# Optimization experiments

Hardware: AMD Instinct MI355X
Metric: run time of the kernel (lower is better)

Reference implementation:

```python
import math
import jax, jax.numpy as jnp
import numpy as np

B, S, DM, H, KH = 2, 2048, 1024, 16, 4
HD = DM // H          # 64
N_REP = H // KH       # 4
ROPE_THETA = 10000.0


def setup_inputs() -> dict:
    key = jax.random.key(0)
    ks = jax.random.split(key, 5)
    x = jax.random.normal(ks[0], (B, S, DM), dtype=jnp.float32)
    wq = jax.random.normal(ks[1], (H * HD, DM), dtype=jnp.float32) * 0.02
    wk = jax.random.normal(ks[2], (KH * HD, DM), dtype=jnp.float32) * 0.02
    wv = jax.random.normal(ks[3], (KH * HD, DM), dtype=jnp.float32) * 0.02
    wo = jax.random.normal(ks[4], (DM, H * HD), dtype=jnp.float32) * 0.02
    # freqs_cis = exp(i * t * theta^(-2j/d)) represented as cos/sin, shape [S, HD//2]
    inv_freq = 1.0 / (ROPE_THETA ** (jnp.arange(0, HD, 2, dtype=jnp.float32) / HD))
    angles = jnp.arange(S, dtype=jnp.float32)[:, None] * inv_freq[None, :]
    return {
        'x': x, 'wq': wq, 'wk': wk, 'wv': wv, 'wo': wo,
        'freqs_cos': jnp.cos(angles), 'freqs_sin': jnp.sin(angles),
    }


def _rope(t, cos, sin):
    # t: [B, S, h, HD]; pairs (even, odd) rotated as complex mul
    tr = t.reshape(*t.shape[:-1], HD // 2, 2)
    xr, xi = tr[..., 0], tr[..., 1]
    c = cos[None, :, None, :]  # [1, S, 1, HD//2]
    s = sin[None, :, None, :]
    out = jnp.stack([xr * c - xi * s, xr * s + xi * c], axis=-1)
    return out.reshape(t.shape)


def reference(x, wq, wk, wv, wo, freqs_cos, freqs_sin):
    b, s, _ = x.shape
    xq = (x @ wq.T).reshape(b, s, H, HD)
    xk = (x @ wk.T).reshape(b, s, KH, HD)
    xv = (x @ wv.T).reshape(b, s, KH, HD)
    xq = _rope(xq, freqs_cos, freqs_sin)
    xk = _rope(xk, freqs_cos, freqs_sin)
    # [B, h, S, HD]
    xq = xq.transpose(0, 2, 1, 3)
    xk = xk.transpose(0, 2, 1, 3)
    xv = xv.transpose(0, 2, 1, 3)
    # GQA: repeat_interleave kv heads to match query heads
    xk = jnp.repeat(xk, N_REP, axis=1)
    xv = jnp.repeat(xv, N_REP, axis=1)
    scale = 1.0 / math.sqrt(HD)
    scores = jnp.einsum('bhqd,bhkd->bhqk', xq, xk) * scale
    causal = jnp.tril(jnp.ones((s, s), dtype=bool))
    scores = jnp.where(causal[None, None], scores, jnp.finfo(scores.dtype).min)
    attn = jax.nn.softmax(scores, axis=-1)
    out = jnp.einsum('bhqk,bhkd->bhqd', attn, xv)
    out = out.transpose(0, 2, 1, 3).reshape(b, s, H * HD)
    return out @ wo.T
```

## Files before the change

### kernel.cpp

```cpp
#include <hip/hip_runtime.h>
#include <hip/hip_bf16.h>
#include <type_traits>

#define B_ 2
#define S_ 2048
#define DM_ 1024
#define H_ 16
#define KH_ 4
#define HD_ 64
#define NREP_ 4
#define QKV_LD 1536
#define CLOG 0.1803368801111244f
#define FIXM 8.0f

typedef float f32x4 __attribute__((ext_vector_type(4)));
typedef float f32x16 __attribute__((ext_vector_type(16)));
typedef short s16x8 __attribute__((ext_vector_type(8)));
typedef unsigned int u32x2 __attribute__((ext_vector_type(2)));

static __device__ __forceinline__ float bf2f(unsigned short u) {
  union { unsigned int u; float f; } x; x.u = ((unsigned int)u) << 16; return x.f;
}
static __device__ __forceinline__ unsigned short f2bf(float f) {
  union { float f; unsigned int u; } x; x.f = f;
  unsigned int r = (x.u + 0x7fffu + ((x.u >> 16) & 1u)) >> 16;
  return (unsigned short)r;
}
static __device__ __forceinline__ unsigned int cvtpk_bf16(float lo, float hi) {
  unsigned int r;
  asm("v_cvt_pk_bf16_f32 %0, %1, %2" : "=v"(r) : "v"(lo), "v"(hi));
  return r;
}
static __device__ __forceinline__ float fexp2(float x) {
  float r;
  asm("v_exp_f32 %0, %1" : "=v"(r) : "v"(x));
  return r;
}

__device__ __forceinline__ void gload_lds16(const unsigned short* g, unsigned short* l) {
  __builtin_amdgcn_global_load_lds(
      (const __attribute__((address_space(1))) unsigned int*)g,
      (__attribute__((address_space(3))) unsigned int*)l, 16, 0, 0);
}

__global__ void cvt_all_k(const float* __restrict__ x,
                          const float* __restrict__ wq, const float* __restrict__ wk,
                          const float* __restrict__ wv, const float* __restrict__ wo,
                          unsigned short* __restrict__ xb,
                          unsigned short* __restrict__ wqkv, unsigned short* __restrict__ wob) {
  int i = (blockIdx.x * 256 + threadIdx.x) * 4;
  const float* src; unsigned short* dst; int off;
  if (i < 4194304)      { src = x;  dst = xb;              off = i; }
  else if (i < 5242880) { src = wq; dst = wqkv;            off = i - 4194304; }
  else if (i < 5505024) { src = wk; dst = wqkv + 1048576;  off = i - 5242880; }
  else if (i < 5767168) { src = wv; dst = wqkv + 1310720;  off = i - 5505024; }
  else                  { src = wo; dst = wob;             off = i - 5767168; }
  float4 v = *(const float4*)(src + off);
  ushort4 o;
  o.x = f2bf(v.x); o.y = f2bf(v.y); o.z = f2bf(v.z); o.w = f2bf(v.w);
  *(ushort4*)(dst + off) = o;
}

#define BM 128
#define BN 128
#define BK 32

template <typename OT>
__global__ __launch_bounds__(512) void gemm_bt(const unsigned short* __restrict__ A,
                                               const unsigned short* __restrict__ Bw,
                                               OT* __restrict__ C,
                                               int M, int N, int K) {
  __shared__ unsigned short lds_a[BM * BK];
  __shared__ unsigned short lds_b[BN * BK];
  const int tid = threadIdx.x;
  const int wave = tid >> 6, lane = tid & 63;
  const int lr = lane & 15, lg = lane >> 4;
  const int m0 = blockIdx.y * BM, n0 = blockIdx.x * BN;
  const int wr = wave >> 2, wc = wave & 3;

  f32x4 acc[4][2] = {};

  const int srow = tid >> 2, scol = (tid & 3) << 3;

  for (int k0 = 0; k0 < K; k0 += BK) {
    gload_lds16(A + (size_t)(m0 + srow) * K + k0 + scol, &lds_a[tid * 8]);
    gload_lds16(Bw + (size_t)(n0 + srow) * K + k0 + scol, &lds_b[tid * 8]);
    __syncthreads();
    s16x8 af[4], bfr[2];
    #pragma unroll
    for (int mi = 0; mi < 4; ++mi)
      af[mi] = *(const s16x8*)&lds_a[(wr * 64 + mi * 16 + lr) * BK + lg * 8];
    #pragma unroll
    for (int ni = 0; ni < 2; ++ni)
      bfr[ni] = *(const s16x8*)&lds_b[(wc * 32 + ni * 16 + lr) * BK + lg * 8];
    #pragma unroll
    for (int mi = 0; mi < 4; ++mi) {
      #pragma unroll
      for (int ni = 0; ni < 2; ++ni)
        acc[mi][ni] = __builtin_amdgcn_mfma_f32_16x16x32_bf16(af[mi], bfr[ni], acc[mi][ni], 0, 0, 0);
    }
    __syncthreads();
  }
  #pragma unroll
  for (int mi = 0; mi < 4; ++mi) {
    #pragma unroll
    for (int ni = 0; ni < 2; ++ni) {
      #pragma unroll
      for (int r = 0; r < 4; ++r) {
        int row = m0 + wr * 64 + mi * 16 + lg * 4 + r;
        int col = n0 + wc * 32 + ni * 16 + lr;
        if constexpr (std::is_same<OT, unsigned short>::value)
          C[(size_t)row * N + col] = f2bf(acc[mi][ni][r]);
        else
          C[(size_t)row * N + col] = acc[mi][ni][r];
      }
    }
  }
}

__global__ void kvpack_k(const unsigned short* __restrict__ qkv,
                         const float* __restrict__ fc, const float* __restrict__ fs,
                         unsigned short* __restrict__ kp, unsigned short* __restrict__ vp) {
  int idx = blockIdx.x * 256 + threadIdx.x;
  int lane = idx & 63;
  int f  = (idx >> 6) & 3;
  int t  = (idx >> 8) & 63;
  int p  = idx >> 14;
  int b = p >> 2, kh = p & 3;
  int ql = lane & 31, hi = lane >> 5;
  {
    int s = t * 32 + ql;
    int d0 = f * 16 + hi * 8;
    const unsigned short* src = qkv + (size_t)(b * S_ + s) * QKV_LD + 1024 + kh * HD_ + d0;
    s16x8 v = *(const s16x8*)src;
    int i0 = d0 >> 1;
    float4 c4 = *(const float4*)(fc + s * 32 + i0);
    float4 s4 = *(const float4*)(fs + s * 32 + i0);
    float cc[4] = {c4.x, c4.y, c4.z, c4.w};
    float ss[4] = {s4.x, s4.y, s4.z, s4.w};
    union { s16x8 v; unsigned int w[4]; } o;
    #pragma unroll
    for (int e = 0; e < 4; ++e) {
      float xr = bf2f((unsigned short)v[2 * e]);
      float xi = bf2f((unsigned short)v[2 * e + 1]);
      o.w[e] = cvtpk_bf16(xr * cc[e] - xi * ss[e], xr * ss[e] + xi * cc[e]);
    }
    *(s16x8*)(kp + (size_t)idx * 8) = o.v;
  }
  {
    int d = (f >> 1) * 32 + ql;
    int kv0 = t * 32 + (f & 1) * 16 + hi * 8;
    const unsigned short* src = qkv + (size_t)(b * S_ + kv0) * QKV_LD + 1280 + kh * HD_ + d;
    s16x8 o;
    #pragma unroll
    for (int e = 0; e < 8; ++e) o[e] = (short)src[(size_t)e * QKV_LD];
    *(s16x8*)(vp + (size_t)idx * 8) = o;
  }
}

__global__ __launch_bounds__(256, 4) void attn_fwd13(const unsigned short* __restrict__ qkv,
                                                     const unsigned short* __restrict__ kp,
                                                     const unsigned short* __restrict__ vp,
                                                     const float* __restrict__ fc,
                                                     const float* __restrict__ fs,
                                                     unsigned short* __restrict__ ob) {
  __shared__ float mbuf[64][34];
  const int tid = threadIdx.x;
  const int wave = tid >> 6, lane = tid & 63;
  const int ql = lane & 31;
  const int hi = lane >> 5;
  const int bi = blockIdx.x;
  const int xcd = bi & 7;
  const int b = xcd >> 2, kh = xcd & 3;
  const int j = bi >> 3;
  const int h = kh * NREP_ + (j & 3);
  const int bt = j >> 2;

  int c, t0, t1;
  bool typeA = false, paired = false, doOut;
  if (bt < 32) {
    typeA = true; paired = true;
    c = 63 - bt;
    int T = c + 1;
    t0 = (wave * T) >> 2; t1 = ((wave + 1) * T) >> 2;
    doOut = (wave == 0);
  } else if (bt < 40) {
    paired = true;
    int bb2 = bt - 32;
    c = (wave < 2) ? (16 + bb2) : (31 - bb2);
    int T = c + 1, Th = T >> 1;
    if ((wave & 1) == 0) { t0 = 0;  t1 = Th; } else { t0 = Th; t1 = T; }
    doOut = (wave == 0) || (wave == 2);
  } else {
    c = (bt - 40) * 4 + wave;
    t0 = 0; t1 = c + 1;
    doOut = true;
  }
  const int q = c * 32 + ql;

  const unsigned short* qrow = qkv + (size_t)(b * S_ + q) * QKV_LD + h * HD_;
  s16x8 qf[4];
  #pragma unroll
  for (int ks = 0; ks < 4; ++ks) {
    s16x8 v = *(const s16x8*)(qrow + ks * 16 + hi * 8);
    int i0 = ks * 8 + hi * 4;
    float4 c4 = *(const float4*)(fc + q * 32 + i0);
    float4 s4 = *(const float4*)(fs + q * 32 + i0);
    float cc[4] = {c4.x, c4.y, c4.z, c4.w};
    float ss[4] = {s4.x, s4.y, s4.z, s4.w};
    union { s16x8 v; unsigned int w[4]; } o;
    #pragma unroll
    for (int e = 0; e < 4; ++e) {
      float xr = bf2f((unsigned short)v[2 * e]);
      float xi = bf2f((unsigned short)v[2 * e + 1]);
      o.w[e] = cvtpk_bf16(xr * cc[e] - xi * ss[e], xr * ss[e] + xi * cc[e]);
    }
    qf[ks] = o.v;
  }

  const unsigned short* kpt = kp + ((size_t)(b * KH_ + kh) << 17) + lane * 8;
  const unsigned short* vpt = vp + ((size_t)(b * KH_ + kh) << 17) + lane * 8;

  f32x16 oT0 = {};
  f32x16 oT1 = {};
  float l = 0.f;

  s16x8 ka[4], va[4];

#define LOADK(T) do { \
    const unsigned short* kp_ = kpt + ((size_t)(T) << 11); \
    ka[0] = *(const s16x8*)(kp_);        ka[1] = *(const s16x8*)(kp_ + 512); \
    ka[2] = *(const s16x8*)(kp_ + 1024); ka[3] = *(const s16x8*)(kp_ + 1536); \
  } while (0)
#define LOADV(T) do { \
    const unsigned short* vp_ = vpt + ((size_t)(T) << 11); \
    va[0] = *(const s16x8*)(vp_);        va[1] = *(const s16x8*)(vp_ + 512); \
    va[2] = *(const s16x8*)(vp_ + 1024); va[3] = *(const s16x8*)(vp_ + 1536); \
  } while (0)

  LOADK(t0);
  LOADV(t0);
  for (int t = t0; t < t1; ++t) {
    const bool diag = (t == c);
    const bool more = (t + 1 < t1);
    f32x16 st = {};
    __builtin_amdgcn_s_setprio(1);
    st = __builtin_amdgcn_mfma_f32_32x32x16_bf16(ka[0], qf[0], st, 0, 0, 0);
    st = __builtin_amdgcn_mfma_f32_32x32x16_bf16(ka[1], qf[1], st, 0, 0, 0);
    st = __builtin_amdgcn_mfma_f32_32x32x16_bf16(ka[2], qf[2], st, 0, 0, 0);
    st = __builtin_amdgcn_mfma_f32_32x32x16_bf16(ka[3], qf[3], st, 0, 0, 0);
    __builtin_amdgcn_s_setprio(0);
    if (more) LOADK(t + 1);
    if (diag) {
      #pragma unroll
      for (int r = 0; r < 16; ++r)
        if (((r & 3) + 8 * (r >> 2) + 4 * hi) > ql) st[r] = -1e30f;
    }
    #pragma unroll
    for (int ksv = 0; ksv < 2; ++ksv) {
      float pr[8];
      #pragma unroll
      for (int e = 0; e < 8; ++e)
        pr[e] = fexp2(fmaf(st[ksv * 8 + e], CLOG, -FIXM));
      l += ((pr[0] + pr[1]) + (pr[2] + pr[3])) + ((pr[4] + pr[5]) + (pr[6] + pr[7]));
      unsigned int a01 = cvtpk_bf16(pr[0], pr[1]);
      unsigned int a23 = cvtpk_bf16(pr[2], pr[3]);
      unsigned int b45 = cvtpk_bf16(pr[4], pr[5]);
      unsigned int b67 = cvtpk_bf16(pr[6], pr[7]);
      asm volatile("v_permlane32_swap_b32 %0, %1" : "+v"(a01), "+v"(b45));
      asm volatile("v_permlane32_swap_b32 %0, %1" : "+v"(a23), "+v"(b67));
      union { s16x8 v; unsigned int w[4]; } pb;
      pb.w[0] = a01; pb.w[1] = a23; pb.w[2] = b45; pb.w[3] = b67;
      __builtin_amdgcn_s_setprio(1);
      oT0 = __builtin_amdgcn_mfma_f32_32x32x16_bf16(va[ksv], pb.v, oT0, 0, 0, 0);
      oT1 = __builtin_amdgcn_mfma_f32_32x32x16_bf16(va[2 + ksv], pb.v, oT1, 0, 0, 0);
      __builtin_amdgcn_s_setprio(0);
    }
    if (more) LOADV(t + 1);
  }
#undef LOADK
#undef LOADV

#define WRITEP do { float* mp_ = &mbuf[lane][0]; \
    _Pragma("unroll") for (int r = 0; r < 16; ++r) { mp_[r] = oT0[r]; mp_[16 + r] = oT1[r]; } \
    mp_[32] = l; } while (0)
#define MERGEP do { float* mp_ = &mbuf[lane][0]; \
    l += mp_[32]; \
    _Pragma("unroll") for (int r = 0; r < 16; ++r) { \
      oT0[r] += mp_[r]; \
      oT1[r] += mp_[16 + r]; } } while (0)

  __syncthreads();
  if (paired && wave == 1) WRITEP;
  __syncthreads();
  if (paired && wave == 0) MERGEP;
  __syncthreads();
  if (paired && wave == 3) WRITEP;
  __syncthreads();
  if (paired && wave == 2) MERGEP;
  __syncthreads();
  if (typeA && wave == 2) WRITEP;
  __syncthreads();
  if (typeA && wave == 0) MERGEP;
#undef WRITEP
#undef MERGEP

  if (doOut) {
    float l_tot = l + __shfl_xor(l, 32);
    float invl = 1.0f / l_tot;
    unsigned short* orow = ob + (size_t)(b * S_ + q) * DM_ + h * HD_;
    #pragma unroll
    for (int dblk = 0; dblk < 2; ++dblk) {
      #pragma unroll
      for (int g = 0; g < 4; ++g) {
        float e0 = (dblk ? oT1[4 * g + 0] : oT0[4 * g + 0]) * invl;
        float e1 = (dblk ? oT1[4 * g + 1] : oT0[4 * g + 1]) * invl;
        float e2 = (dblk ? oT1[4 * g + 2] : oT0[4 * g + 2]) * invl;
        float e3 = (dblk ? oT1[4 * g + 3] : oT0[4 * g + 3]) * invl;
        u32x2 w;
        w.x = cvtpk_bf16(e0, e1);
        w.y = cvtpk_bf16(e2, e3);
        *(u32x2*)(orow + dblk * 32 + g * 8 + 4 * hi) = w;
      }
    }
  }
}

extern "C" void kernel_launch(void* const* d_in, const int* in_sizes, int n_in,
                              void* d_out, int out_size, void* d_ws, size_t ws_size,
                              hipStream_t stream) {
  const float* x  = (const float*)d_in[0];
  const float* wq = (const float*)d_in[1];
  const float* wk = (const float*)d_in[2];
  const float* wv = (const float*)d_in[3];
  const float* wo = (const float*)d_in[4];
  const float* fc = (const float*)d_in[5];
  const float* fs = (const float*)d_in[6];
  float* out = (float*)d_out;

  const size_t nX    = (size_t)B_ * S_ * DM_;
  const size_t nWQKV = (size_t)QKV_LD * DM_;
  const size_t nWO   = (size_t)DM_ * DM_;
  const size_t nQKV  = (size_t)B_ * S_ * QKV_LD;
  const size_t nKV   = (size_t)B_ * S_ * KH_ * HD_;

  unsigned short* xb    = (unsigned short*)d_ws;
  unsigned short* wqkv  = xb + nX;
  unsigned short* wob   = wqkv + nWQKV;
  unsigned short* qkv   = wob + nWO;
  unsigned short* kpk   = qkv + nQKV;
  unsigned short* vpk   = kpk + nKV;
  unsigned short* a_buf = vpk + nKV;

  const int M = B_ * S_;

  cvt_all_k<<<6656, 256, 0, stream>>>(x, wq, wk, wv, wo, xb, wqkv, wob);

  gemm_bt<unsigned short><<<dim3(QKV_LD / BN, M / BM), 512, 0, stream>>>(
      xb, wqkv, qkv, M, QKV_LD, DM_);

  kvpack_k<<<512, 256, 0, stream>>>(qkv, fc, fs, kpk, vpk);

  attn_fwd13<<<1408, 256, 0, stream>>>(qkv, kpk, vpk, fc, fs, a_buf);

  gemm_bt<float><<<dim3(DM_ / BN, M / BM), 512, 0, stream>>>(
      a_buf, wob, out, M, DM_, DM_);
}
```

Before: 99.52 us.

## Double-buffer GEMM tiles and process two query heads per attention block

```diff
diff --git a/kernel.cpp b/kernel.cpp
--- a/kernel.cpp
+++ b/kernel.cpp
@@ -61,54 +61,64 @@
   *(ushort4*)(dst + off) = o;
 }
 
-#define BM 128
+#define BM 64
 #define BN 128
 #define BK 32
 
 template <typename OT>
-__global__ __launch_bounds__(512) void gemm_bt(const unsigned short* __restrict__ A,
+__global__ __launch_bounds__(256) void gemm_bt(const unsigned short* __restrict__ A,
                                                const unsigned short* __restrict__ Bw,
                                                OT* __restrict__ C,
                                                int M, int N, int K) {
-  __shared__ unsigned short lds_a[BM * BK];
-  __shared__ unsigned short lds_b[BN * BK];
+  __shared__ unsigned short lds_a[2][BM * BK];
+  __shared__ unsigned short lds_b[2][BN * BK];
   const int tid = threadIdx.x;
   const int wave = tid >> 6, lane = tid & 63;
   const int lr = lane & 15, lg = lane >> 4;
   const int m0 = blockIdx.y * BM, n0 = blockIdx.x * BN;
-  const int wr = wave >> 2, wc = wave & 3;
-
-  f32x4 acc[4][2] = {};
+  const int wr = wave >> 1, wc = wave & 1;
+
+  f32x4 acc[2][4] = {};
 
   const int srow = tid >> 2, scol = (tid & 3) << 3;
 
+#define STAGE(k0, bufi) do { \
+    gload_lds16(A + (size_t)(m0 + srow) * K + (k0) + scol, &lds_a[bufi][tid * 8]); \
+    gload_lds16(Bw + (size_t)(n0 + srow) * K + (k0) + scol, &lds_b[bufi][tid * 8]); \
+    gload_lds16(Bw + (size_t)(n0 + 64 + srow) * K + (k0) + scol, &lds_b[bufi][2048 + tid * 8]); \
+  } while (0)
+
+  STAGE(0, 0);
+  __syncthreads();
+  int cur = 0;
   for (int k0 = 0; k0 < K; k0 += BK) {
-    gload_lds16(A + (size_t)(m0 + srow) * K + k0 + scol, &lds_a[tid * 8]);
-    gload_lds16(Bw + (size_t)(n0 + srow) * K + k0 + scol, &lds_b[tid * 8]);
+    if (k0 + BK < K) STAGE(k0 + BK, cur ^ 1);
+    s16x8 af[2], bfr[4];
+    #pragma unroll
+    for (int mi = 0; mi < 2; ++mi)
+      af[mi] = *(const s16x8*)&lds_a[cur][(wr * 32 + mi * 16 + lr) * BK + lg * 8];
+    #pragma unroll
+    for (int ni = 0; ni < 4; ++ni)
+      bfr[ni] = *(const s16x8*)&lds_b[cur][(wc * 64 + ni * 16 + lr) * BK + lg * 8];
+    #pragma unroll
+    for (int mi = 0; mi < 2; ++mi) {
+      #pragma unroll
+      for (int ni = 0; ni < 4; ++ni)
+        acc[mi][ni] = __builtin_amdgcn_mfma_f32_16x16x32_bf16(af[mi], bfr[ni], acc[mi][ni], 0, 0, 0);
+    }
     __syncthreads();
-    s16x8 af[4], bfr[2];
-    #pragma unroll
-    for (int mi = 0; mi < 4; ++mi)
-      af[mi] = *(const s16x8*)&lds_a[(wr * 64 + mi * 16 + lr) * BK + lg * 8];
-    #pragma unroll
-    for (int ni = 0; ni < 2; ++ni)
-      bfr[ni] = *(const s16x8*)&lds_b[(wc * 32 + ni * 16 + lr) * BK + lg * 8];
-    #pragma unroll
-    for (int mi = 0; mi < 4; ++mi) {
-      #pragma unroll
-      for (int ni = 0; ni < 2; ++ni)
-        acc[mi][ni] = __builtin_amdgcn_mfma_f32_16x16x32_bf16(af[mi], bfr[ni], acc[mi][ni], 0, 0, 0);
-    }
-    __syncthreads();
-  }
+    cur ^= 1;
+  }
+#undef STAGE
+
   #pragma unroll
-  for (int mi = 0; mi < 4; ++mi) {
-    #pragma unroll
-    for (int ni = 0; ni < 2; ++ni) {
+  for (int mi = 0; mi < 2; ++mi) {
+    #pragma unroll
+    for (int ni = 0; ni < 4; ++ni) {
       #pragma unroll
       for (int r = 0; r < 4; ++r) {
-        int row = m0 + wr * 64 + mi * 16 + lg * 4 + r;
-        int col = n0 + wc * 32 + ni * 16 + lr;
+        int row = m0 + wr * 32 + mi * 16 + lg * 4 + r;
+        int col = n0 + wc * 64 + ni * 16 + lr;
         if constexpr (std::is_same<OT, unsigned short>::value)
           C[(size_t)row * N + col] = f2bf(acc[mi][ni][r]);
         else
@@ -158,12 +168,12 @@
   }
 }
 
-__global__ __launch_bounds__(256, 4) void attn_fwd13(const unsigned short* __restrict__ qkv,
-                                                     const unsigned short* __restrict__ kp,
-                                                     const unsigned short* __restrict__ vp,
-                                                     const float* __restrict__ fc,
-                                                     const float* __restrict__ fs,
-                                                     unsigned short* __restrict__ ob) {
+__global__ __launch_bounds__(256) void attn_fwd16(const unsigned short* __restrict__ qkv,
+                                                  const unsigned short* __restrict__ kp,
+                                                  const unsigned short* __restrict__ vp,
+                                                  const float* __restrict__ fc,
+                                                  const float* __restrict__ fs,
+                                                  unsigned short* __restrict__ ob) {
   __shared__ float mbuf[64][34];
   const int tid = threadIdx.x;
   const int wave = tid >> 6, lane = tid & 63;
@@ -173,8 +183,9 @@
   const int xcd = bi & 7;
   const int b = xcd >> 2, kh = xcd & 3;
   const int j = bi >> 3;
-  const int h = kh * NREP_ + (j & 3);
-  const int bt = j >> 2;
+  const int h0 = kh * NREP_ + (j & 1) * 2;
+  const int h1 = h0 + 1;
+  const int bt = j >> 1;
 
   int c, t0, t1;
   bool typeA = false, paired = false, doOut;
@@ -198,32 +209,37 @@
   }
   const int q = c * 32 + ql;
 
-  const unsigned short* qrow = qkv + (size_t)(b * S_ + q) * QKV_LD + h * HD_;
-  s16x8 qf[4];
+  const unsigned short* qrow0 = qkv + (size_t)(b * S_ + q) * QKV_LD + h0 * HD_;
+  s16x8 qf0[4], qf1[4];
   #pragma unroll
   for (int ks = 0; ks < 4; ++ks) {
-    s16x8 v = *(const s16x8*)(qrow + ks * 16 + hi * 8);
+    s16x8 v0 = *(const s16x8*)(qrow0 + ks * 16 + hi * 8);
+    s16x8 v1 = *(const s16x8*)(qrow0 + HD_ + ks * 16 + hi * 8);
     int i0 = ks * 8 + hi * 4;
     float4 c4 = *(const float4*)(fc + q * 32 + i0);
     float4 s4 = *(const float4*)(fs + q * 32 + i0);
     float cc[4] = {c4.x, c4.y, c4.z, c4.w};
     float ss[4] = {s4.x, s4.y, s4.z, s4.w};
-    union { s16x8 v; unsigned int w[4]; } o;
+    union { s16x8 v; unsigned int w[4]; } o0, o1;
     #pragma unroll
     for (int e = 0; e < 4; ++e) {
-      float xr = bf2f((unsigned short)v[2 * e]);
-      float xi = bf2f((unsigned short)v[2 * e + 1]);
-      o.w[e] = cvtpk_bf16(xr * cc[e] - xi * ss[e], xr * ss[e] + xi * cc[e]);
-    }
-    qf[ks] = o.v;
+      float xr0 = bf2f((unsigned short)v0[2 * e]);
+      float xi0 = bf2f((unsigned short)v0[2 * e + 1]);
+      o0.w[e] = cvtpk_bf16(xr0 * cc[e] - xi0 * ss[e], xr0 * ss[e] + xi0 * cc[e]);
+      float xr1 = bf2f((unsigned short)v1[2 * e]);
+      float xi1 = bf2f((unsigned short)v1[2 * e + 1]);
+      o1.w[e] = cvtpk_bf16(xr1 * cc[e] - xi1 * ss[e], xr1 * ss[e] + xi1 * cc[e]);
+    }
+    qf0[ks] = o0.v;
+    qf1[ks] = o1.v;
   }
 
   const unsigned short* kpt = kp + ((size_t)(b * KH_ + kh) << 17) + lane * 8;
   const unsigned short* vpt = vp + ((size_t)(b * KH_ + kh) << 17) + lane * 8;
 
-  f32x16 oT0 = {};
-  f32x16 oT1 = {};
-  float l = 0.f;
+  f32x16 o00 = {}, o01 = {};
+  f32x16 o10 = {}, o11 = {};
+  float l0 = 0.f, l1 = 0.f;
 
   s16x8 ka[4], va[4];
 
@@ -243,84 +259,122 @@
   for (int t = t0; t < t1; ++t) {
     const bool diag = (t == c);
     const bool more = (t + 1 < t1);
-    f32x16 st = {};
-    __builtin_amdgcn_s_setprio(1);
-    st = __builtin_amdgcn_mfma_f32_32x32x16_bf16(ka[0], qf[0], st, 0, 0, 0);
-    st = __builtin_amdgcn_mfma_f32_32x32x16_bf16(ka[1], qf[1], st, 0, 0, 0);
-    st = __builtin_amdgcn_mfma_f32_32x32x16_bf16(ka[2], qf[2], st, 0, 0, 0);
-    st = __builtin_amdgcn_mfma_f32_32x32x16_bf16(ka[3], qf[3], st, 0, 0, 0);
-    __builtin_amdgcn_s_setprio(0);
+    f32x16 st0 = {}, st1 = {};
+    st0 = __builtin_amdgcn_mfma_f32_32x32x16_bf16(ka[0], qf0[0], st0, 0, 0, 0);
+    st1 = __builtin_amdgcn_mfma_f32_32x32x16_bf16(ka[0], qf1[0], st1, 0, 0, 0);
+    st0 = __builtin_amdgcn_mfma_f32_32x32x16_bf16(ka[1], qf0[1], st0, 0, 0, 0);
+    st1 = __builtin_amdgcn_mfma_f32_32x32x16_bf16(ka[1], qf1[1], st1, 0, 0, 0);
+    st0 = __builtin_amdgcn_mfma_f32_32x32x16_bf16(ka[2], qf0[2], st0, 0, 0, 0);
+    st1 = __builtin_amdgcn_mfma_f32_32x32x16_bf16(ka[2], qf1[2], st1, 0, 0, 0);
+    st0 = __builtin_amdgcn_mfma_f32_32x32x16_bf16(ka[3], qf0[3], st0, 0, 0, 0);
+    st1 = __builtin_amdgcn_mfma_f32_32x32x16_bf16(ka[3], qf1[3], st1, 0, 0, 0);
     if (more) LOADK(t + 1);
     if (diag) {
       #pragma unroll
       for (int r = 0; r < 16; ++r)
-        if (((r & 3) + 8 * (r >> 2) + 4 * hi) > ql) st[r] = -1e30f;
-    }
+        if (((r & 3) + 8 * (r >> 2) + 4 * hi) > ql) { st0[r] = -1e30f; st1[r] = -1e30f; }
+    }
+    unsigned int pw0[8], pw1[8];
     #pragma unroll
     for (int ksv = 0; ksv < 2; ++ksv) {
-      float pr[8];
+      float p0[8], p1[8];
       #pragma unroll
-      for (int e = 0; e < 8; ++e)
-        pr[e] = fexp2(fmaf(st[ksv * 8 + e], CLOG, -FIXM));
-      l += ((pr[0] + pr[1]) + (pr[2] + pr[3])) + ((pr[4] + pr[5]) + (pr[6] + pr[7]));
-      unsigned int a01 = cvtpk_bf16(pr[0], pr[1]);
-      unsigned int a23 = cvtpk_bf16(pr[2], pr[3]);
-      unsigned int b45 = cvtpk_bf16(pr[4], pr[5]);
-      unsigned int b67 = cvtpk_bf16(pr[6], pr[7]);
-      asm volatile("v_permlane32_swap_b32 %0, %1" : "+v"(a01), "+v"(b45));
-      asm volatile("v_permlane32_swap_b32 %0, %1" : "+v"(a23), "+v"(b67));
-      union { s16x8 v; unsigned int w[4]; } pb;
-      pb.w[0] = a01; pb.w[1] = a23; pb.w[2] = b45; pb.w[3] = b67;
-      __builtin_amdgcn_s_setprio(1);
-      oT0 = __builtin_amdgcn_mfma_f32_32x32x16_bf16(va[ksv], pb.v, oT0, 0, 0, 0);
-      oT1 = __builtin_amdgcn_mfma_f32_32x32x16_bf16(va[2 + ksv], pb.v, oT1, 0, 0, 0);
-      __builtin_amdgcn_s_setprio(0);
+      for (int e = 0; e < 8; ++e) {
+        p0[e] = fexp2(fmaf(st0[ksv * 8 + e], CLOG, -FIXM));
+        p1[e] = fexp2(fmaf(st1[ksv * 8 + e], CLOG, -FIXM));
+      }
+      l0 += ((p0[0] + p0[1]) + (p0[2] + p0[3])) + ((p0[4] + p0[5]) + (p0[6] + p0[7]));
+      l1 += ((p1[0] + p1[1]) + (p1[2] + p1[3])) + ((p1[4] + p1[5]) + (p1[6] + p1[7]));
+      unsigned int a0 = cvtpk_bf16(p0[0], p0[1]), a1 = cvtpk_bf16(p0[2], p0[3]);
+      unsigned int a2 = cvtpk_bf16(p0[4], p0[5]), a3 = cvtpk_bf16(p0[6], p0[7]);
+      unsigned int b0 = cvtpk_bf16(p1[0], p1[1]), b1 = cvtpk_bf16(p1[2], p1[3]);
+      unsigned int b2 = cvtpk_bf16(p1[4], p1[5]), b3 = cvtpk_bf16(p1[6], p1[7]);
+      asm volatile("v_permlane32_swap_b32 %0, %1" : "+v"(a0), "+v"(a2));
+      asm volatile("v_permlane32_swap_b32 %0, %1" : "+v"(a1), "+v"(a3));
+      asm volatile("v_permlane32_swap_b32 %0, %1" : "+v"(b0), "+v"(b2));
+      asm volatile("v_permlane32_swap_b32 %0, %1" : "+v"(b1), "+v"(b3));
+      pw0[ksv * 4 + 0] = a0; pw0[ksv * 4 + 1] = a1; pw0[ksv * 4 + 2] = a2; pw0[ksv * 4 + 3] = a3;
+      pw1[ksv * 4 + 0] = b0; pw1[ksv * 4 + 1] = b1; pw1[ksv * 4 + 2] = b2; pw1[ksv * 4 + 3] = b3;
+    }
+    #pragma unroll
+    for (int ksv = 0; ksv < 2; ++ksv) {
+      union { s16x8 v; unsigned int w[4]; } pb0, pb1;
+      pb0.w[0] = pw0[ksv * 4 + 0]; pb0.w[1] = pw0[ksv * 4 + 1];
+      pb0.w[2] = pw0[ksv * 4 + 2]; pb0.w[3] = pw0[ksv * 4 + 3];
+      pb1.w[0] = pw1[ksv * 4 + 0]; pb1.w[1] = pw1[ksv * 4 + 1];
+      pb1.w[2] = pw1[ksv * 4 + 2]; pb1.w[3] = pw1[ksv * 4 + 3];
+      o00 = __builtin_amdgcn_mfma_f32_32x32x16_bf16(va[ksv], pb0.v, o00, 0, 0, 0);
+      o10 = __builtin_amdgcn_mfma_f32_32x32x16_bf16(va[ksv], pb1.v, o10, 0, 0, 0);
+      o01 = __builtin_amdgcn_mfma_f32_32x32x16_bf16(va[2 + ksv], pb0.v, o01, 0, 0, 0);
+      o11 = __builtin_amdgcn_mfma_f32_32x32x16_bf16(va[2 + ksv], pb1.v, o11, 0, 0, 0);
     }
     if (more) LOADV(t + 1);
   }
 #undef LOADK
 #undef LOADV
 
-#define WRITEP do { float* mp_ = &mbuf[lane][0]; \
-    _Pragma("unroll") for (int r = 0; r < 16; ++r) { mp_[r] = oT0[r]; mp_[16 + r] = oT1[r]; } \
-    mp_[32] = l; } while (0)
-#define MERGEP do { float* mp_ = &mbuf[lane][0]; \
-    l += mp_[32]; \
+#define WRITEP(OA, OB, L) do { float* mp_ = &mbuf[lane][0]; \
+    _Pragma("unroll") for (int r = 0; r < 16; ++r) { mp_[r] = OA[r]; mp_[16 + r] = OB[r]; } \
+    mp_[32] = L; } while (0)
+#define MERGEP(OA, OB, L) do { float* mp_ = &mbuf[lane][0]; \
+    L += mp_[32]; \
     _Pragma("unroll") for (int r = 0; r < 16; ++r) { \
-      oT0[r] += mp_[r]; \
-      oT1[r] += mp_[16 + r]; } } while (0)
-
-  __syncthreads();
-  if (paired && wave == 1) WRITEP;
-  __syncthreads();
-  if (paired && wave == 0) MERGEP;
-  __syncthreads();
-  if (paired && wave == 3) WRITEP;
-  __syncthreads();
-  if (paired && wave == 2) MERGEP;
-  __syncthreads();
-  if (typeA && wave == 2) WRITEP;
-  __syncthreads();
-  if (typeA && wave == 0) MERGEP;
+      OA[r] += mp_[r]; \
+      OB[r] += mp_[16 + r]; } } while (0)
+
+  __syncthreads();
+  if (paired && wave == 1) WRITEP(o00, o01, l0);
+  __syncthreads();
+  if (paired && wave == 0) MERGEP(o00, o01, l0);
+  __syncthreads();
+  if (paired && wave == 3) WRITEP(o00, o01, l0);
+  __syncthreads();
+  if (paired && wave == 2) MERGEP(o00, o01, l0);
+  __syncthreads();
+  if (typeA && wave == 2) WRITEP(o00, o01, l0);
+  __syncthreads();
+  if (typeA && wave == 0) MERGEP(o00, o01, l0);
+  __syncthreads();
+  if (paired && wave == 1) WRITEP(o10, o11, l1);
+  __syncthreads();
+  if (paired && wave == 0) MERGEP(o10, o11, l1);
+  __syncthreads();
+  if (paired && wave == 3) WRITEP(o10, o11, l1);
+  __syncthreads();
+  if (paired && wave == 2) MERGEP(o10, o11, l1);
+  __syncthreads();
+  if (typeA && wave == 2) WRITEP(o10, o11, l1);
+  __syncthreads();
+  if (typeA && wave == 0) MERGEP(o10, o11, l1);
 #undef WRITEP
 #undef MERGEP
 
   if (doOut) {
-    float l_tot = l + __shfl_xor(l, 32);
-    float invl = 1.0f / l_tot;
-    unsigned short* orow = ob + (size_t)(b * S_ + q) * DM_ + h * HD_;
+    float lt0 = l0 + __shfl_xor(l0, 32);
+    float lt1 = l1 + __shfl_xor(l1, 32);
+    float il0 = 1.0f / lt0;
+    float il1 = 1.0f / lt1;
+    unsigned short* orow = ob + (size_t)(b * S_ + q) * DM_ + h0 * HD_;
     #pragma unroll
     for (int dblk = 0; dblk < 2; ++dblk) {
       #pragma unroll
       for (int g = 0; g < 4; ++g) {
-        float e0 = (dblk ? oT1[4 * g + 0] : oT0[4 * g + 0]) * invl;
-        float e1 = (dblk ? oT1[4 * g + 1] : oT0[4 * g + 1]) * invl;
-        float e2 = (dblk ? oT1[4 * g + 2] : oT0[4 * g + 2]) * invl;
-        float e3 = (dblk ? oT1[4 * g + 3] : oT0[4 * g + 3]) * invl;
+        float e0 = (dblk ? o01[4 * g + 0] : o00[4 * g + 0]) * il0;
+        float e1 = (dblk ? o01[4 * g + 1] : o00[4 * g + 1]) * il0;
+        float e2 = (dblk ? o01[4 * g + 2] : o00[4 * g + 2]) * il0;
+        float e3 = (dblk ? o01[4 * g + 3] : o00[4 * g + 3]) * il0;
         u32x2 w;
         w.x = cvtpk_bf16(e0, e1);
         w.y = cvtpk_bf16(e2, e3);
         *(u32x2*)(orow + dblk * 32 + g * 8 + 4 * hi) = w;
+        float f0 = (dblk ? o11[4 * g + 0] : o10[4 * g + 0]) * il1;
+        float f1 = (dblk ? o11[4 * g + 1] : o10[4 * g + 1]) * il1;
+        float f2 = (dblk ? o11[4 * g + 2] : o10[4 * g + 2]) * il1;
+        float f3 = (dblk ? o11[4 * g + 3] : o10[4 * g + 3]) * il1;
+        u32x2 w2;
+        w2.x = cvtpk_bf16(f0, f1);
+        w2.y = cvtpk_bf16(f2, f3);
+        *(u32x2*)(orow + HD_ + dblk * 32 + g * 8 + 4 * hi) = w2;
       }
     }
   }
@@ -356,13 +410,13 @@
 
   cvt_all_k<<<6656, 256, 0, stream>>>(x, wq, wk, wv, wo, xb, wqkv, wob);
 
-  gemm_bt<unsigned short><<<dim3(QKV_LD / BN, M / BM), 512, 0, stream>>>(
+  gemm_bt<unsigned short><<<dim3(QKV_LD / BN, M / BM), 256, 0, stream>>>(
       xb, wqkv, qkv, M, QKV_LD, DM_);
 
   kvpack_k<<<512, 256, 0, stream>>>(qkv, fc, fs, kpk, vpk);
 
-  attn_fwd13<<<1408, 256, 0, stream>>>(qkv, kpk, vpk, fc, fs, a_buf);
-
-  gemm_bt<float><<<dim3(DM_ / BN, M / BM), 512, 0, stream>>>(
+  attn_fwd16<<<704, 256, 0, stream>>>(qkv, kpk, vpk, fc, fs, a_buf);
+
+  gemm_bt<float><<<dim3(DM_ / BN, M / BM), 256, 0, stream>>>(
       a_buf, wob, out, M, DM_, DM_);
 }
```

Result: slower. 114.7 us (+15.2%).
